# Optimization experiments

Hardware: AMD Instinct MI355X
Metric: run time of the kernel (lower is better)

The kernel has to match this reference:

```python
import jax, jax.numpy as jnp
import numpy as np

N = 100_000
E = 3_200_000
NCLASS = 64
TOPK = 16
NHID = 128
DEGREE = 6


def setup_inputs() -> dict:
    key = jax.random.key(0)
    ks = jax.random.split(key, 8)
    x = jax.random.normal(ks[0], (N, NCLASS), dtype=jnp.float32)
    edge_row = jax.random.randint(ks[1], (E,), 0, N, dtype=jnp.int64)
    edge_col = jax.random.randint(ks[2], (E,), 0, N, dtype=jnp.int64)
    edge_val = jax.random.uniform(ks[3], (E,), dtype=jnp.float32) / 32.0  # ~row-normalized
    # torch.nn.Linear init: U(-1/sqrt(fan_in), 1/sqrt(fan_in))
    lim1 = 1.0 / np.sqrt(TOPK)
    lim2 = 1.0 / np.sqrt(NHID)
    W1 = jax.random.uniform(ks[4], (NHID, TOPK), jnp.float32, -lim1, lim1)
    b1 = jnp.zeros((NHID,), jnp.float32)
    W2 = jax.random.uniform(ks[5], (DEGREE, NHID), jnp.float32, -lim2, lim2)
    b2 = jnp.zeros((DEGREE,), jnp.float32)
    return {"x": x, "edge_row": edge_row, "edge_col": edge_col,
            "edge_val": edge_val, "W1": W1, "b1": b1, "W2": W2, "b2": b2}


def _spmm(edge_row, edge_col, edge_val, h):
    # (adj @ h)[i] = sum_{(i,j) in E} val_ij * h[j]
    return jax.ops.segment_sum(edge_val[:, None] * h[edge_col], edge_row,
                               num_segments=N)


def reference(x, edge_row, edge_col, edge_val, W1, b1, W2, b2):
    # gating: softmax over classes -> top-k probs -> small MLP -> hop weights
    p = jax.nn.softmax(x, axis=1)
    tk, _ = jax.lax.top_k(p, TOPK)                       # [N, TOPK]
    h = jax.nn.leaky_relu(tk @ W1.T + b1, 0.1)           # [N, NHID]
    weight = jax.nn.softmax(h @ W2.T + b2, axis=1)       # [N, DEGREE]
    # dropout is identity in eval mode
    out = weight[:, 0:1] * x
    cur = x
    for i in range(DEGREE - 1):
        cur = _spmm(edge_row, edge_col, edge_val, cur)
        out = out + weight[:, i + 1:i + 2] * cur
    return jax.nn.log_softmax(out, axis=1)
```

## Files before the change

kernel.cpp:

```cpp
#include <hip/hip_runtime.h>
#include <math.h>

#define N_NODES 100000
#define N_EDGES 3200000
#define NCLASS  64
#define TOPK    16
#define NHID    128
#define DEG     6

#define NBUCK   391
#define NSEG    8
#define SEGCAP  1408

__device__ __forceinline__ float bf2f(unsigned short u) {
    return __uint_as_float(((unsigned)u) << 16);
}
__device__ __forceinline__ unsigned short f2bf(float f) {
    unsigned u = __float_as_uint(f);
    u = (u + 0x7FFFu + ((u >> 16) & 1u)) >> 16;
    return (unsigned short)u;
}

__device__ __forceinline__ float wave_max(float v) {
    #pragma unroll
    for (int off = 1; off < 64; off <<= 1) v = fmaxf(v, __shfl_xor(v, off));
    return v;
}
__device__ __forceinline__ float wave_sum(float v) {
    #pragma unroll
    for (int off = 1; off < 64; off <<= 1) v += __shfl_xor(v, off);
    return v;
}

__global__ void phase1_bucket(const int* __restrict__ erow, const int* __restrict__ ecol,
                              const float* __restrict__ eval, int* __restrict__ fill,
                              int2* __restrict__ staging) {
    unsigned xcc;
    asm("s_getreg_b32 %0, hwreg(HW_REG_XCC_ID)" : "=s"(xcc));
    int s = (int)(xcc & 7u);
    int i = blockIdx.x * 256 + threadIdx.x;
    if (i < N_EDGES) {
        int r = __builtin_nontemporal_load(&erow[i]);
        int c = __builtin_nontemporal_load(&ecol[i]);
        float w = __builtin_nontemporal_load(&eval[i]);
        int b = r >> 8;
        int pos = atomicAdd(&fill[(s * NBUCK + b) * 16], 1);
        if (pos < SEGCAP) {
            int2 e;
            e.x = (c << 8) | (r & 255);
            e.y = __float_as_int(w);
            staging[((size_t)b * NSEG + s) * SEGCAP + pos] = e;
        }
    }
}

__global__ void bucket_scan(const int* __restrict__ fill, int* __restrict__ bucket_base,
                            int* __restrict__ row_ptr) {
    __shared__ int sdat[512];
    int tid = threadIdx.x;
    int c = 0;
    if (tid < NBUCK) {
        #pragma unroll
        for (int s = 0; s < NSEG; s++) c += min(fill[(s * NBUCK + tid) * 16], SEGCAP);
    }
    sdat[tid] = c;
    __syncthreads();
    for (int off = 1; off < 512; off <<= 1) {
        int t = (tid >= off) ? sdat[tid - off] : 0;
        __syncthreads();
        sdat[tid] += t;
        __syncthreads();
    }
    if (tid < NBUCK) bucket_base[tid] = sdat[tid] - c;
    if (tid == 0) row_ptr[N_NODES] = sdat[511];
}

__global__ __launch_bounds__(256) void phase2_build(
        const int2* __restrict__ staging, const int* __restrict__ fill,
        const int* __restrict__ bucket_base, int* __restrict__ row_ptr,
        int2* __restrict__ edges_s) {
    __shared__ int lhist[256];
    __shared__ int lscan[256];
    __shared__ int lfill[256];
    __shared__ int sseg[NSEG];
    int b = blockIdx.x, tid = threadIdx.x;
    lhist[tid] = 0;
    if (tid < NSEG) sseg[tid] = min(fill[(tid * NBUCK + b) * 16], SEGCAP);
    __syncthreads();
    for (int s = 0; s < NSEG; s++) {
        int c = sseg[s];
        const int2* seg = staging + ((size_t)b * NSEG + s) * SEGCAP;
        for (int j = tid; j < c; j += 256) atomicAdd(&lhist[seg[j].x & 255], 1);
    }
    __syncthreads();
    int v = lhist[tid];
    lscan[tid] = v;
    __syncthreads();
    for (int off = 1; off < 256; off <<= 1) {
        int t = (tid >= off) ? lscan[tid - off] : 0;
        __syncthreads();
        lscan[tid] += t;
        __syncthreads();
    }
    int base_b = bucket_base[b];
    int excl = base_b + (lscan[tid] - v);
    int grow = b * 256 + tid;
    if (grow < N_NODES) row_ptr[grow] = excl;
    lfill[tid] = excl;
    __syncthreads();
    for (int s = 0; s < NSEG; s++) {
        int c = sseg[s];
        const int2* seg = staging + ((size_t)b * NSEG + s) * SEGCAP;
        for (int j = tid; j < c; j += 256) {
            int2 e = seg[j];
            int rl = e.x & 255;
            int pos = atomicAdd(&lfill[rl], 1);
            edges_s[pos] = make_int2((int)(((unsigned)e.x) >> 8), e.y);
        }
    }
}

#define GNODES 32
__global__ __launch_bounds__(256) void gating_kernel(
        const float* __restrict__ x,  const float* __restrict__ W1,
        const float* __restrict__ b1, const float* __restrict__ W2,
        const float* __restrict__ b2, float* __restrict__ weight,
        float* __restrict__ out_acc, unsigned short* __restrict__ xbf) {
    __shared__ float sW1t[TOPK * NHID];
    __shared__ float sb1[NHID];
    __shared__ float sW2[DEG * NHID];
    __shared__ float sb2[DEG];
    int tid = threadIdx.x;
    for (int idx = tid; idx < NHID * TOPK; idx += 256) {
        int k = idx / NHID, j = idx - k * NHID;
        sW1t[idx] = W1[j * TOPK + k];
    }
    for (int i = tid; i < NHID; i += 256) sb1[i] = b1[i];
    for (int i = tid; i < DEG * NHID; i += 256) sW2[i] = W2[i];
    if (tid < DEG) sb2[tid] = b2[tid];
    __syncthreads();

    int wave = tid >> 6;
    int lane = tid & 63;

    for (int it = 0; it < GNODES / 4; it++) {
        int node = blockIdx.x * GNODES + it * 4 + wave;
        if (node >= N_NODES) continue;

        float xv = x[node * NCLASS + lane];
        xbf[node * NCLASS + lane] = f2bf(xv);

        float v = xv;
        #pragma unroll
        for (int k = 2; k <= 64; k <<= 1) {
            #pragma unroll
            for (int j = k >> 1; j > 0; j >>= 1) {
                float o = __shfl_xor(v, j);
                bool keep_small = (((lane & j) == 0) == ((lane & k) == 0));
                v = keep_small ? fminf(v, o) : fmaxf(v, o);
            }
        }
        float m = __shfl(v, 63);
        float e = __expf(v - m);
        float s = wave_sum(e);
        float inv_s = 1.0f / s;

        float h0 = sb1[lane], h1 = sb1[lane + 64];
        #pragma unroll
        for (int k = 0; k < TOPK; k++) {
            float sv = __shfl(v, 63 - k);
            float tk = __expf(sv - m) * inv_s;
            h0 += tk * sW1t[k * NHID + lane];
            h1 += tk * sW1t[k * NHID + lane + 64];
        }
        h0 = (h0 > 0.f) ? h0 : 0.1f * h0;
        h1 = (h1 > 0.f) ? h1 : 0.1f * h1;

        float w[DEG];
        float wm = -1e30f;
        #pragma unroll
        for (int d = 0; d < DEG; d++) {
            float part = h0 * sW2[d * NHID + lane] + h1 * sW2[d * NHID + lane + 64];
            w[d] = wave_sum(part) + sb2[d];
            wm = fmaxf(wm, w[d]);
        }
        float wsum = 0.f;
        #pragma unroll
        for (int d = 0; d < DEG; d++) { w[d] = __expf(w[d] - wm); wsum += w[d]; }
        float inv = 1.0f / wsum;

        if (lane < DEG) weight[node * DEG + lane] = w[lane] * inv;
        out_acc[node * NCLASS + lane] = w[0] * inv * xv;
    }
}

__global__ __launch_bounds__(256) void spmm_kernel(
        const unsigned short* __restrict__ src, unsigned short* __restrict__ dst,
        const int* __restrict__ row_ptr, const int2* __restrict__ edges_s,
        const float* __restrict__ weight,
        float* __restrict__ out_acc, float* __restrict__ final_out,
        int hop, int is_last) {
    int wave = threadIdx.x >> 6;
    int lane = threadIdx.x & 63;
    int node = blockIdx.x * 4 + wave;
    if (node >= N_NODES) return;

    int start = __builtin_amdgcn_readfirstlane(row_ptr[node]);
    int end   = __builtin_amdgcn_readfirstlane(row_ptr[node + 1]);

    const long long* edq = (const long long*)edges_s;
    float acc = 0.f;
    int e = start;
    for (; e + 8 <= end; e += 8) {
        long long q[8];
        #pragma unroll
        for (int k = 0; k < 8; k++) q[k] = __builtin_nontemporal_load(&edq[e + k]);
        float vv[8], ff[8];
        #pragma unroll
        for (int k = 0; k < 8; k++) {
            int col = __builtin_amdgcn_readfirstlane((int)(unsigned)q[k]);
            vv[k] = __int_as_float(__builtin_amdgcn_readfirstlane((int)(q[k] >> 32)));
            ff[k] = bf2f(src[col * NCLASS + lane]);
        }
        #pragma unroll
        for (int k = 0; k < 8; k++) acc += vv[k] * ff[k];
    }
    for (; e < end; e++) {
        long long q0 = __builtin_nontemporal_load(&edq[e]);
        int   c0 = __builtin_amdgcn_readfirstlane((int)(unsigned)q0);
        float v0 = __int_as_float(__builtin_amdgcn_readfirstlane((int)(q0 >> 32)));
        acc += v0 * bf2f(src[c0 * NCLASS + lane]);
    }

    float w = weight[node * DEG + hop];
    if (!is_last) {
        dst[node * NCLASS + lane] = f2bf(acc);
        out_acc[node * NCLASS + lane] += w * acc;
    } else {
        float v = out_acc[node * NCLASS + lane] + w * acc;
        float m = wave_max(v);
        float e2 = __expf(v - m);
        float s = wave_sum(e2);
        final_out[node * NCLASS + lane] = v - m - __logf(s);
    }
}

extern "C" void kernel_launch(void* const* d_in, const int* in_sizes, int n_in,
                              void* d_out, int out_size, void* d_ws, size_t ws_size,
                              hipStream_t stream) {
    const float* x    = (const float*)d_in[0];
    const int*   erow = (const int*)  d_in[1];
    const int*   ecol = (const int*)  d_in[2];
    const float* eval = (const float*)d_in[3];
    const float* W1   = (const float*)d_in[4];
    const float* b1   = (const float*)d_in[5];
    const float* W2   = (const float*)d_in[6];
    const float* b2   = (const float*)d_in[7];
    float* out = (float*)d_out;

    char* ws = (char*)d_ws;
    size_t off = 0;
    auto alloc = [&](size_t bytes) -> void* {
        void* p = ws + off;
        off = (off + bytes + 255) & ~(size_t)255;
        return p;
    };
    char* regionA = (char*)alloc((size_t)N_NODES * NCLASS * 2 * 3);
    int2* staging = (int2*)regionA;
    unsigned short* xbf  = (unsigned short*)regionA;
    unsigned short* cur0 = (unsigned short*)(regionA + (size_t)N_NODES * NCLASS * 2);
    unsigned short* cur1 = (unsigned short*)(regionA + (size_t)N_NODES * NCLASS * 4);

    int2*  edges_s     = (int2*)alloc((size_t)N_EDGES * 8);
    int*   row_ptr     = (int*) alloc((size_t)(N_NODES + 1) * 4);
    int*   fill        = (int*) alloc((size_t)NSEG * NBUCK * 16 * 4);
    int*   bucket_base = (int*) alloc((size_t)NBUCK * 4);
    float* weight      = (float*)alloc((size_t)N_NODES * DEG * 4);

    const int EB = (N_EDGES + 255) / 256;
    const int WB = (N_NODES + 3) / 4;
    const int GB = (N_NODES + GNODES - 1) / GNODES;

    hipMemsetAsync(fill, 0, (size_t)NSEG * NBUCK * 16 * 4, stream);
    phase1_bucket<<<EB, 256, 0, stream>>>(erow, ecol, eval, fill, staging);
    bucket_scan<<<1, 512, 0, stream>>>(fill, bucket_base, row_ptr);
    phase2_build<<<NBUCK, 256, 0, stream>>>(staging, fill, bucket_base, row_ptr, edges_s);

    gating_kernel<<<GB, 256, 0, stream>>>(x, W1, b1, W2, b2, weight, out, xbf);

    spmm_kernel<<<WB, 256, 0, stream>>>(xbf,  cur0, row_ptr, edges_s, weight, out, out, 1, 0);
    spmm_kernel<<<WB, 256, 0, stream>>>(cur0, cur1, row_ptr, edges_s, weight, out, out, 2, 0);
    spmm_kernel<<<WB, 256, 0, stream>>>(cur1, cur0, row_ptr, edges_s, weight, out, out, 3, 0);
    spmm_kernel<<<WB, 256, 0, stream>>>(cur0, cur1, row_ptr, edges_s, weight, out, out, 4, 0);
    spmm_kernel<<<WB, 256, 0, stream>>>(cur1, cur0, row_ptr, edges_s, weight, out, out, 5, 1);
}
```

Baseline: 775.1 us.

## Batch bucket scatter through LDS and process two rows per wave in SpMM

The edge bucketing kernel now stages edges in shared memory per bucket and flushes them in groups of 8 with one global atomic per group. This replaces one global atomic per edge and spreads writes over a single contiguous segment per bucket instead of per-XCC segments. The SpMM kernel now has each wave handle two adjacent rows with interleaved 4-edge gathers, giving more independent loads in flight and reusing the shared row_ptr read. The batching loop adds block-wide barriers on every iteration. Rows with uneven lengths drain one after the other, which can leave a wave underused.

```diff
diff --git a/kernel.cpp b/kernel.cpp
--- a/kernel.cpp
+++ b/kernel.cpp
@@ -9,8 +9,9 @@
 #define DEG     6
 
 #define NBUCK   391
-#define NSEG    8
-#define SEGCAP  1408
+#define BUCKCAP 9216
+#define P1_NWG  512
+#define P1_CHUNK ((N_EDGES + P1_NWG - 1) / P1_NWG)
 
 __device__ __forceinline__ float bf2f(unsigned short u) {
     return __uint_as_float(((unsigned)u) << 16);
@@ -32,24 +33,61 @@
     return v;
 }
 
-__global__ void phase1_bucket(const int* __restrict__ erow, const int* __restrict__ ecol,
-                              const float* __restrict__ eval, int* __restrict__ fill,
-                              int2* __restrict__ staging) {
-    unsigned xcc;
-    asm("s_getreg_b32 %0, hwreg(HW_REG_XCC_ID)" : "=s"(xcc));
-    int s = (int)(xcc & 7u);
-    int i = blockIdx.x * 256 + threadIdx.x;
-    if (i < N_EDGES) {
-        int r = __builtin_nontemporal_load(&erow[i]);
-        int c = __builtin_nontemporal_load(&ecol[i]);
-        float w = __builtin_nontemporal_load(&eval[i]);
-        int b = r >> 8;
-        int pos = atomicAdd(&fill[(s * NBUCK + b) * 16], 1);
-        if (pos < SEGCAP) {
-            int2 e;
-            e.x = (c << 8) | (r & 255);
-            e.y = __float_as_int(w);
-            staging[((size_t)b * NSEG + s) * SEGCAP + pos] = e;
+__global__ __launch_bounds__(256) void phase1_bucket(
+        const int* __restrict__ erow, const int* __restrict__ ecol,
+        const float* __restrict__ eval, int* __restrict__ fill,
+        int2* __restrict__ staging) {
+    __shared__ int2 buf[NBUCK][8];
+    __shared__ int  lcnt[NBUCK];
+    int tid = threadIdx.x;
+    int wv = tid >> 6, lane = tid & 63;
+    for (int b = tid; b < NBUCK; b += 256) lcnt[b] = 0;
+    __syncthreads();
+
+    int base  = blockIdx.x * P1_CHUNK;
+    int limit = min(base + P1_CHUNK, N_EDGES);
+    int i = base + tid;
+    bool have = false;
+    int2 ed = make_int2(0, 0);
+    int  eb = 0;
+
+    while (true) {
+        if (!have && i < limit) {
+            int   r = __builtin_nontemporal_load(&erow[i]);
+            int   c = __builtin_nontemporal_load(&ecol[i]);
+            float w = __builtin_nontemporal_load(&eval[i]);
+            ed.x = (c << 8) | (r & 255);
+            ed.y = __float_as_int(w);
+            eb = r >> 8;
+            i += 256;
+            have = true;
+        }
+        if (have) {
+            int p = atomicAdd(&lcnt[eb], 1);
+            if (p < 8) { buf[eb][p] = ed; have = false; }
+        }
+        int pending = __syncthreads_count((int)(have || (i < limit)));
+        for (int b = wv; b < NBUCK; b += 4) {
+            if (lcnt[b] >= 8) {
+                int pos = 0;
+                if (lane == 0) pos = atomicAdd(&fill[b * 16], 8);
+                pos = __shfl(pos, 0);
+                if (lane < 8)
+                    staging[(size_t)b * BUCKCAP + pos + lane] = buf[b][lane];
+                if (lane == 0) lcnt[b] = 0;
+            }
+        }
+        __syncthreads();
+        if (pending == 0) break;
+    }
+    for (int b = wv; b < NBUCK; b += 4) {
+        int c = lcnt[b];
+        if (c > 0) {
+            int pos = 0;
+            if (lane == 0) pos = atomicAdd(&fill[b * 16], c);
+            pos = __shfl(pos, 0);
+            if (lane < c)
+                staging[(size_t)b * BUCKCAP + pos + lane] = buf[b][lane];
         }
     }
 }
@@ -59,10 +97,7 @@
     __shared__ int sdat[512];
     int tid = threadIdx.x;
     int c = 0;
-    if (tid < NBUCK) {
-        #pragma unroll
-        for (int s = 0; s < NSEG; s++) c += min(fill[(s * NBUCK + tid) * 16], SEGCAP);
-    }
+    if (tid < NBUCK) c = min(fill[tid * 16], BUCKCAP);
     sdat[tid] = c;
     __syncthreads();
     for (int off = 1; off < 512; off <<= 1) {
@@ -82,16 +117,12 @@
     __shared__ int lhist[256];
     __shared__ int lscan[256];
     __shared__ int lfill[256];
-    __shared__ int sseg[NSEG];
     int b = blockIdx.x, tid = threadIdx.x;
+    int c = min(fill[b * 16], BUCKCAP);
+    const int2* seg = staging + (size_t)b * BUCKCAP;
     lhist[tid] = 0;
-    if (tid < NSEG) sseg[tid] = min(fill[(tid * NBUCK + b) * 16], SEGCAP);
-    __syncthreads();
-    for (int s = 0; s < NSEG; s++) {
-        int c = sseg[s];
-        const int2* seg = staging + ((size_t)b * NSEG + s) * SEGCAP;
-        for (int j = tid; j < c; j += 256) atomicAdd(&lhist[seg[j].x & 255], 1);
-    }
+    __syncthreads();
+    for (int j = tid; j < c; j += 256) atomicAdd(&lhist[seg[j].x & 255], 1);
     __syncthreads();
     int v = lhist[tid];
     lscan[tid] = v;
@@ -102,21 +133,16 @@
         lscan[tid] += t;
         __syncthreads();
     }
-    int base_b = bucket_base[b];
-    int excl = base_b + (lscan[tid] - v);
+    int excl = bucket_base[b] + (lscan[tid] - v);
     int grow = b * 256 + tid;
     if (grow < N_NODES) row_ptr[grow] = excl;
     lfill[tid] = excl;
     __syncthreads();
-    for (int s = 0; s < NSEG; s++) {
-        int c = sseg[s];
-        const int2* seg = staging + ((size_t)b * NSEG + s) * SEGCAP;
-        for (int j = tid; j < c; j += 256) {
-            int2 e = seg[j];
-            int rl = e.x & 255;
-            int pos = atomicAdd(&lfill[rl], 1);
-            edges_s[pos] = make_int2((int)(((unsigned)e.x) >> 8), e.y);
-        }
+    for (int j = tid; j < c; j += 256) {
+        int2 e = seg[j];
+        int rl = e.x & 255;
+        int pos = atomicAdd(&lfill[rl], 1);
+        edges_s[pos] = make_int2((int)(((unsigned)e.x) >> 8), e.y);
     }
 }
 
@@ -194,6 +220,41 @@
     }
 }
 
+__device__ __forceinline__ void gather4(const unsigned short* __restrict__ src,
+                                        const long long* __restrict__ edq,
+                                        int e, int lane, float& acc) {
+    long long q0 = __builtin_nontemporal_load(&edq[e]);
+    long long q1 = __builtin_nontemporal_load(&edq[e + 1]);
+    long long q2 = __builtin_nontemporal_load(&edq[e + 2]);
+    long long q3 = __builtin_nontemporal_load(&edq[e + 3]);
+    int c0 = __builtin_amdgcn_readfirstlane((int)(unsigned)q0);
+    int c1 = __builtin_amdgcn_readfirstlane((int)(unsigned)q1);
+    int c2 = __builtin_amdgcn_readfirstlane((int)(unsigned)q2);
+    int c3 = __builtin_amdgcn_readfirstlane((int)(unsigned)q3);
+    float v0 = __int_as_float(__builtin_amdgcn_readfirstlane((int)(q0 >> 32)));
+    float v1 = __int_as_float(__builtin_amdgcn_readfirstlane((int)(q1 >> 32)));
+    float v2 = __int_as_float(__builtin_amdgcn_readfirstlane((int)(q2 >> 32)));
+    float v3 = __int_as_float(__builtin_amdgcn_readfirstlane((int)(q3 >> 32)));
+    float f0 = bf2f(src[c0 * NCLASS + lane]);
+    float f1 = bf2f(src[c1 * NCLASS + lane]);
+    float f2 = bf2f(src[c2 * NCLASS + lane]);
+    float f3 = bf2f(src[c3 * NCLASS + lane]);
+    acc += v0 * f0; acc += v1 * f1; acc += v2 * f2; acc += v3 * f3;
+}
+
+__device__ __forceinline__ float drain_row(const unsigned short* __restrict__ src,
+                                           const long long* __restrict__ edq,
+                                           int e, int end, int lane, float acc) {
+    for (; e + 4 <= end; e += 4) gather4(src, edq, e, lane, acc);
+    for (; e < end; e++) {
+        long long q0 = __builtin_nontemporal_load(&edq[e]);
+        int   c0 = __builtin_amdgcn_readfirstlane((int)(unsigned)q0);
+        float v0 = __int_as_float(__builtin_amdgcn_readfirstlane((int)(q0 >> 32)));
+        acc += v0 * bf2f(src[c0 * NCLASS + lane]);
+    }
+    return acc;
+}
+
 __global__ __launch_bounds__(256) void spmm_kernel(
         const unsigned short* __restrict__ src, unsigned short* __restrict__ dst,
         const int* __restrict__ row_ptr, const int2* __restrict__ edges_s,
@@ -202,46 +263,45 @@
         int hop, int is_last) {
     int wave = threadIdx.x >> 6;
     int lane = threadIdx.x & 63;
-    int node = blockIdx.x * 4 + wave;
-    if (node >= N_NODES) return;
-
-    int start = __builtin_amdgcn_readfirstlane(row_ptr[node]);
-    int end   = __builtin_amdgcn_readfirstlane(row_ptr[node + 1]);
+    int wid = blockIdx.x * 4 + wave;
+    int rA = wid * 2;
+    if (rA >= N_NODES) return;
+    int rB = rA + 1;
+
+    int sA   = __builtin_amdgcn_readfirstlane(row_ptr[rA]);
+    int endA = __builtin_amdgcn_readfirstlane(row_ptr[rA + 1]);
+    int endB = __builtin_amdgcn_readfirstlane(row_ptr[rA + 2]);
 
     const long long* edq = (const long long*)edges_s;
-    float acc = 0.f;
-    int e = start;
-    for (; e + 8 <= end; e += 8) {
-        long long q[8];
-        #pragma unroll
-        for (int k = 0; k < 8; k++) q[k] = __builtin_nontemporal_load(&edq[e + k]);
-        float vv[8], ff[8];
-        #pragma unroll
-        for (int k = 0; k < 8; k++) {
-            int col = __builtin_amdgcn_readfirstlane((int)(unsigned)q[k]);
-            vv[k] = __int_as_float(__builtin_amdgcn_readfirstlane((int)(q[k] >> 32)));
-            ff[k] = bf2f(src[col * NCLASS + lane]);
-        }
-        #pragma unroll
-        for (int k = 0; k < 8; k++) acc += vv[k] * ff[k];
-    }
-    for (; e < end; e++) {
-        long long q0 = __builtin_nontemporal_load(&edq[e]);
-        int   c0 = __builtin_amdgcn_readfirstlane((int)(unsigned)q0);
-        float v0 = __int_as_float(__builtin_amdgcn_readfirstlane((int)(q0 >> 32)));
-        acc += v0 * bf2f(src[c0 * NCLASS + lane]);
-    }
-
-    float w = weight[node * DEG + hop];
+    float accA = 0.f, accB = 0.f;
+    int eA = sA, eB = endA;
+    while (eA + 4 <= endA && eB + 4 <= endB) {
+        gather4(src, edq, eA, lane, accA);
+        gather4(src, edq, eB, lane, accB);
+        eA += 4; eB += 4;
+    }
+    accA = drain_row(src, edq, eA, endA, lane, accA);
+    accB = drain_row(src, edq, eB, endB, lane, accB);
+
+    float wA = weight[rA * DEG + hop];
+    float wB = weight[rB * DEG + hop];
     if (!is_last) {
-        dst[node * NCLASS + lane] = f2bf(acc);
-        out_acc[node * NCLASS + lane] += w * acc;
+        dst[rA * NCLASS + lane] = f2bf(accA);
+        dst[rB * NCLASS + lane] = f2bf(accB);
+        out_acc[rA * NCLASS + lane] += wA * accA;
+        out_acc[rB * NCLASS + lane] += wB * accB;
     } else {
-        float v = out_acc[node * NCLASS + lane] + w * acc;
-        float m = wave_max(v);
-        float e2 = __expf(v - m);
-        float s = wave_sum(e2);
-        final_out[node * NCLASS + lane] = v - m - __logf(s);
+        float vA = out_acc[rA * NCLASS + lane] + wA * accA;
+        float mA = wave_max(vA);
+        float eA2 = __expf(vA - mA);
+        float sA2 = wave_sum(eA2);
+        final_out[rA * NCLASS + lane] = vA - mA - __logf(sA2);
+
+        float vB = out_acc[rB * NCLASS + lane] + wB * accB;
+        float mB = wave_max(vB);
+        float eB2 = __expf(vB - mB);
+        float sB2 = wave_sum(eB2);
+        final_out[rB * NCLASS + lane] = vB - mB - __logf(sB2);
     }
 }
 
@@ -273,16 +333,15 @@
 
     int2*  edges_s     = (int2*)alloc((size_t)N_EDGES * 8);
     int*   row_ptr     = (int*) alloc((size_t)(N_NODES + 1) * 4);
-    int*   fill        = (int*) alloc((size_t)NSEG * NBUCK * 16 * 4);
+    int*   fill        = (int*) alloc((size_t)NBUCK * 16 * 4);
     int*   bucket_base = (int*) alloc((size_t)NBUCK * 4);
     float* weight      = (float*)alloc((size_t)N_NODES * DEG * 4);
 
-    const int EB = (N_EDGES + 255) / 256;
-    const int WB = (N_NODES + 3) / 4;
+    const int WB = ((N_NODES / 2) + 3) / 4;
     const int GB = (N_NODES + GNODES - 1) / GNODES;
 
-    hipMemsetAsync(fill, 0, (size_t)NSEG * NBUCK * 16 * 4, stream);
-    phase1_bucket<<<EB, 256, 0, stream>>>(erow, ecol, eval, fill, staging);
+    hipMemsetAsync(fill, 0, (size_t)NBUCK * 16 * 4, stream);
+    phase1_bucket<<<P1_NWG, 256, 0, stream>>>(erow, ecol, eval, fill, staging);
     bucket_scan<<<1, 512, 0, stream>>>(fill, bucket_base, row_ptr);
     phase2_build<<<NBUCK, 256, 0, stream>>>(staging, fill, bucket_base, row_ptr, edges_s);
 
```

After: 935.1 us. +20.7%, slower.
